# Kernel optimization log

Measured on AMD Instinct MI355X. Metric: run time of the kernel, lower is better.

The kernel has to match this reference:

```python
import jax, jax.numpy as jnp
import numpy as np

H = 8            # num heads
K_ORDER = 3      # polynomial filter order


def setup_inputs() -> dict:
    key = jax.random.key(0)
    ks = jax.random.split(key, 7)
    B, N, D = 4, 2048, 256
    s = 0.05  # weight scale to keep softmax/poly numerically tame
    x = jax.random.normal(ks[0], (B, N, D), jnp.float32)
    Wq = jax.random.normal(ks[1], (D, D), jnp.float32) * s
    Wk = jax.random.normal(ks[2], (D, D), jnp.float32) * s
    Wv = jax.random.normal(ks[3], (D, D), jnp.float32) * s
    Wo = jax.random.normal(ks[4], (D, D), jnp.float32) * s
    coeffs = jax.random.normal(ks[5], (H, K_ORDER + 1), jnp.float32) * 0.5
    z = jnp.zeros((D,), jnp.float32)
    return {"x": x, "Wq": Wq, "bq": z, "Wk": Wk, "bk": z,
            "Wv": Wv, "bv": z, "Wo": Wo, "bo": z, "coeffs": coeffs}


def reference(x, Wq, bq, Wk, bk, Wv, bv, Wo, bo, coeffs):
    B, N, D = x.shape
    hd = D // H

    def split_heads(t):  # [B,N,D] -> [B,H,N,hd]
        return t.reshape(B, N, H, hd).transpose(0, 2, 1, 3)

    q = split_heads(x @ Wq + bq)
    k = split_heads(x @ Wk + bk)
    v = split_heads(x @ Wv + bv)

    # Estimator: learned adjacency via scaled-dot-product softmax, [B,H,N,N]
    scale = jnp.asarray(1.0 / np.sqrt(hd), x.dtype)
    A = jax.nn.softmax(jnp.einsum('bhnd,bhmd->bhnm', q, k) * scale, axis=-1)

    # Filter: X' = sum_{k=0}^{K} c[h,k] * A^k V
    out = coeffs[None, :, 0, None, None] * v
    t = v
    for kk in range(1, K_ORDER + 1):
        t = jnp.einsum('bhnm,bhmd->bhnd', A, t)
        out = out + coeffs[None, :, kk, None, None] * t

    merged = out.transpose(0, 2, 1, 3).reshape(B, N, D)  # concat heads
    return merged @ Wo + bo
```

## Files before the change

kernel.cpp:

```cpp
#include <hip/hip_runtime.h>
#include <hip/hip_bf16.h>

typedef __hip_bfloat16 bf16;
typedef __attribute__((ext_vector_type(8))) short short8;
typedef __attribute__((ext_vector_type(4))) short short4v;
typedef __attribute__((ext_vector_type(4))) float f32x4;

#define BB 4
#define NN 2048
#define DD 256
#define HH 8
#define HD 32
#define BN (BB*NN)
#define ELEMS (BN*DD)

__device__ int g_isf32;
__device__ __attribute__((aligned(256))) unsigned short g_xb [ELEMS];
__device__ __attribute__((aligned(256))) unsigned short g_qb [ELEMS];
__device__ __attribute__((aligned(256))) unsigned short g_kb [ELEMS];
__device__ __attribute__((aligned(256))) unsigned short g_tA [ELEMS];
__device__ __attribute__((aligned(256))) unsigned short g_tB [ELEMS];
__device__ __attribute__((aligned(256))) float          g_acc[ELEMS];
__device__ __attribute__((aligned(256))) unsigned short g_mg [ELEMS];
__device__ __attribute__((aligned(256))) unsigned short g_wt [4*DD*DD];
__device__ __attribute__((aligned(256))) float g_bias[4*DD];
__device__ __attribute__((aligned(256))) float g_cf[HH*4];
__device__ __attribute__((aligned(256))) float g_invl[BB*HH*NN];

__device__ __forceinline__ float b2f(unsigned short u) {
    union { unsigned int i; float f; } c; c.i = ((unsigned int)u) << 16; return c.f;
}
__device__ __forceinline__ unsigned short f2b(float f) {
    bf16 h = __float2bfloat16(f);
    return *reinterpret_cast<unsigned short*>(&h);
}
#if __has_builtin(__builtin_amdgcn_cvt_pk_bf16_f32)
typedef __attribute__((ext_vector_type(2))) __bf16 bf16x2t;
__device__ __forceinline__ unsigned int pk2(float a, float b) {
    union { bf16x2t v; unsigned int u; } c;
    c.v = __builtin_amdgcn_cvt_pk_bf16_f32(a, b);
    return c.u;
}
#else
__device__ __forceinline__ unsigned int pk2(float a, float b) {
    unsigned int ua = __float_as_uint(a), ub = __float_as_uint(b);
    ua = (ua + 0x7FFFu + ((ua >> 16) & 1u)) >> 16;
    ub = (ub + 0x7FFFu + ((ub >> 16) & 1u)) & 0xFFFF0000u;
    return ua | ub;
}
#endif
__device__ __forceinline__ float ldin(const void* p, int i, int f32m) {
    return f32m ? ((const float*)p)[i] : b2f(((const unsigned short*)p)[i]);
}

__global__ __launch_bounds__(256) void probe_kernel(const void* __restrict__ x)
{
    __shared__ int cnt;
    if (threadIdx.x == 0) cnt = 0;
    __syncthreads();
    const unsigned short* u = (const unsigned short*)x;
    int w = 0;
    for (int i = threadIdx.x; i < 1024; i += 256) {
        const int e = (u[2 * i] >> 7) & 0xFF;
        if (e < 100 || e > 140) ++w;
    }
    atomicAdd(&cnt, w);
    __syncthreads();
    if (threadIdx.x == 0) g_isf32 = (cnt > 300) ? 1 : 0;
}

__global__ __launch_bounds__(256) void prep_x_kernel(const void* __restrict__ x)
{
    const int f32m = g_isf32;
    const size_t i0 = ((size_t)blockIdx.x * 256 + threadIdx.x) * 8;
    if (f32m) {
        const float4 a = *(const float4*)((const float*)x + i0);
        const float4 b = *(const float4*)((const float*)x + i0 + 4);
        union { uint4 v; unsigned int u[4]; } o;
        o.u[0] = pk2(a.x, a.y); o.u[1] = pk2(a.z, a.w);
        o.u[2] = pk2(b.x, b.y); o.u[3] = pk2(b.z, b.w);
        *(uint4*)(g_xb + i0) = o.v;
    } else {
        *(uint4*)(g_xb + i0) = *(const uint4*)((const unsigned short*)x + i0);
    }
}

__global__ __launch_bounds__(256) void prep_w_kernel(
    const void* W0, const void* W1, const void* W2, const void* W3,
    const void* bq, const void* bk, const void* bv, const void* bo,
    const void* coeffs)
{
    const int f32m = g_isf32;
    __shared__ unsigned short tile[64][65];
    const int mat = blockIdx.y;
    const void* W = (mat == 0) ? W0 : (mat == 1) ? W1 : (mat == 2) ? W2 : W3;
    const int k0 = (blockIdx.x >> 2) * 64;
    const int n0 = (blockIdx.x & 3) * 64;
    const int t  = threadIdx.x;

    if (blockIdx.x == 0 && blockIdx.y == 0) {
        g_bias[0 * DD + t] = ldin(bq, t, f32m);
        g_bias[1 * DD + t] = ldin(bk, t, f32m);
        g_bias[2 * DD + t] = ldin(bv, t, f32m);
        g_bias[3 * DD + t] = ldin(bo, t, f32m);
        if (t < 32) g_cf[t] = ldin(coeffs, t, f32m);
    }

    #pragma unroll
    for (int it = 0; it < 16; ++it) {
        const int flat = it * 256 + t;
        const int i = flat >> 6, j = flat & 63;
        tile[j][i] = f2b(ldin(W, (k0 + i) * DD + n0 + j, f32m));
    }
    __syncthreads();
    unsigned short* wt = g_wt + mat * DD * DD;
    #pragma unroll
    for (int it = 0; it < 16; ++it) {
        const int flat = it * 256 + t;
        const int nl = flat >> 6, kl = flat & 63;
        wt[(n0 + nl) * DD + k0 + kl] = tile[nl][kl];
    }
}

__global__ __launch_bounds__(256) void qkv_gemm_kernel()
{
    __shared__ unsigned short xs[128 * 32];
    __shared__ unsigned short wl[64 * 32];
    const int t  = threadIdx.x;
    const int w  = t >> 6, l = t & 63, lg = l >> 4, ln = l & 15;
    const int wm = w >> 1, wn = w & 1;
    const int r0 = blockIdx.x * 128;
    const int n0 = blockIdx.y * 64;
    const int mat = blockIdx.z;
    const unsigned short* wt = g_wt + mat * DD * DD;

    f32x4 acc[4][2];
    #pragma unroll
    for (int m = 0; m < 4; ++m)
        #pragma unroll
        for (int s = 0; s < 2; ++s) acc[m][s] = (f32x4){0,0,0,0};

    for (int kc = 0; kc < DD; kc += 32) {
        __syncthreads();
        #pragma unroll
        for (int c = 0; c < 2; ++c) {
            const int s = c * 256 + t;
            *(uint4*)(xs + (s >> 2) * 32 + (s & 3) * 8) =
                *(const uint4*)(g_xb + (size_t)(r0 + (s >> 2)) * DD + kc + (s & 3) * 8);
        }
        *(uint4*)(wl + (t >> 2) * 32 + (t & 3) * 8) =
            *(const uint4*)(wt + (size_t)(n0 + (t >> 2)) * DD + kc + (t & 3) * 8);
        __syncthreads();

        short8 af[4];
        #pragma unroll
        for (int m = 0; m < 4; ++m)
            af[m] = *(const short8*)(xs + (wm * 64 + m * 16 + ln) * 32 + lg * 8);
        #pragma unroll
        for (int s = 0; s < 2; ++s) {
            const short8 bfr = *(const short8*)(wl + (wn * 32 + s * 16 + ln) * 32 + lg * 8);
            #pragma unroll
            for (int m = 0; m < 4; ++m)
                acc[m][s] = __builtin_amdgcn_mfma_f32_16x16x32_bf16(af[m], bfr, acc[m][s], 0, 0, 0);
        }
    }

    const float QS = 0.17677669529663687f * 1.4426950408889634f;
    #pragma unroll
    for (int s = 0; s < 2; ++s) {
        const int j = n0 + wn * 32 + s * 16 + ln;
        const float bias = g_bias[mat * DD + j];
        const int h = j >> 5, dd = j & 31;
        #pragma unroll
        for (int m = 0; m < 4; ++m) {
            #pragma unroll
            for (int r = 0; r < 4; ++r) {
                const int rn = r0 + wm * 64 + m * 16 + lg * 4 + r;
                const int b = rn >> 11, n = rn & (NN - 1);
                const int bh = b * HH + h;
                const float val = acc[m][s][r] + bias;
                if (mat == 0) {
                    g_qb[((size_t)bh * NN + n) * HD + dd] = f2b(val * QS);
                } else if (mat == 1) {
                    g_kb[((size_t)bh * NN + n) * HD + dd] = f2b(val);
                } else {
                    g_tA[((size_t)bh * HD + dd) * NN + n] = f2b(val);
                    g_acc[(size_t)rn * DD + j] = g_cf[h * 4] * val;
                }
            }
        }
    }
}

#define KSP 40
#define TSP 136
template<int KIND>
__global__ __launch_bounds__(512, 1) void attn_pass_kernel(const int kidx, const int dir)
{
    __shared__ unsigned short ks[128 * KSP];
    __shared__ unsigned short ts[32 * TSP];

    const unsigned short* __restrict__ tin  = dir ? g_tB : g_tA;
    unsigned short*       __restrict__ tout = dir ? g_tA : g_tB;

    const int tid = threadIdx.x;
    const int w   = tid >> 6;
    const int l   = tid & 63;
    const int lg  = l >> 4;
    const int ln  = l & 15;

    const int bi = blockIdx.x;
    const int bh = (bi & 7) * 4 + ((bi >> 3) & 3);
    const int qt = bi >> 5;
    const int h  = bh & (HH - 1);
    const int b  = bh >> 3;
    const int q0 = qt * 128;
    const int qw = q0 + w * 16;

    const short8 qf = *(const short8*)(g_qb +
        ((size_t)bh * NN + qw + ln) * HD + lg * 8);

    const unsigned short* kb = g_kb + (size_t)bh * NN * HD;
    const unsigned short* tb = tin  + (size_t)bh * HD * NN;

    const f32x4 zero = {0.f, 0.f, 0.f, 0.f};
    f32x4 oacc0 = zero, oacc1 = zero;
    float lsum = 0.f;

    const int krow = tid >> 2, kcol = (tid & 3) * 8;
    const int trow = tid >> 4, tcol = (tid & 15) * 8;

    for (int it = 0; it < 16; ++it) {
        const int k0 = it * 128;
        __syncthreads();
        *(uint4*)(ks + krow * KSP + kcol) =
            *(const uint4*)(kb + (size_t)k0 * HD + tid * 8);
        *(uint4*)(ts + trow * TSP + tcol) =
            *(const uint4*)(tb + (size_t)trow * NN + k0 + tcol);
        __syncthreads();

        #pragma unroll
        for (int c = 0; c < 8; ++c) {
            const short8 kf = *(const short8*)(ks + (c * 16 + ln) * KSP + lg * 8);
            f32x4 s = __builtin_amdgcn_mfma_f32_16x16x32_bf16(kf, qf, zero, 0, 0, 0);
            float p[4];
            #pragma unroll
            for (int r = 0; r < 4; ++r) p[r] = __builtin_amdgcn_exp2f(s[r]);
            if (KIND == 0) lsum += p[0] + p[1] + p[2] + p[3];
            union { unsigned int u[2]; short4v s4; } pb;
            pb.u[0] = pk2(p[0], p[1]); pb.u[1] = pk2(p[2], p[3]);
            const short4v tf0 = *(const short4v*)(ts + ln * TSP + c * 16 + lg * 4);
            const short4v tf1 = *(const short4v*)(ts + (16 + ln) * TSP + c * 16 + lg * 4);
            oacc0 = __builtin_amdgcn_mfma_f32_16x16x16bf16_1k(tf0, pb.s4, oacc0, 0, 0, 0);
            oacc1 = __builtin_amdgcn_mfma_f32_16x16x16bf16_1k(tf1, pb.s4, oacc1, 0, 0, 0);
        }
    }

    float invl;
    if (KIND == 0) {
        lsum += __shfl_xor(lsum, 16, 64);
        lsum += __shfl_xor(lsum, 32, 64);
        invl = 1.0f / lsum;
        if (lg == 0) g_invl[(size_t)bh * NN + qw + ln] = invl;
    } else {
        invl = g_invl[(size_t)bh * NN + qw + ln];
    }

    const float ck = g_cf[h * 4 + kidx];
    #pragma unroll
    for (int hf = 0; hf < 2; ++hf) {
        const f32x4& oa = hf ? oacc1 : oacc0;
        #pragma unroll
        for (int r = 0; r < 4; ++r) {
            const int d = hf * 16 + lg * 4 + r;
            const float val = oa[r] * invl;
            const size_t gi = ((size_t)(b * NN + qw + ln)) * DD + h * HD + d;
            if (KIND != 2) {
                tout[((size_t)bh * HD + d) * NN + qw + ln] = f2b(val);
                g_acc[gi] += ck * val;
            } else {
                g_mg[gi] = f2b(g_acc[gi] + ck * val);
            }
        }
    }
}

__global__ __launch_bounds__(256) void out_gemm_kernel(void* __restrict__ out)
{
    __shared__ unsigned short xs[64 * 32];
    __shared__ unsigned short wl[64 * 32];
    const int f32m = g_isf32;
    const int t  = threadIdx.x;
    const int w  = t >> 6, l = t & 63, lg = l >> 4, ln = l & 15;
    const int r0 = blockIdx.x * 64;
    const int n0 = blockIdx.y * 64;
    const unsigned short* wt = g_wt + 3 * DD * DD;
    const int sr = t >> 2, sc = (t & 3) * 8;

    f32x4 acc[4] = {{0,0,0,0},{0,0,0,0},{0,0,0,0},{0,0,0,0}};

    for (int kc = 0; kc < DD; kc += 32) {
        __syncthreads();
        *(uint4*)(xs + sr * 32 + sc) =
            *(const uint4*)(g_mg + (size_t)(r0 + sr) * DD + kc + sc);
        *(uint4*)(wl + sr * 32 + sc) =
            *(const uint4*)(wt + (size_t)(n0 + sr) * DD + kc + sc);
        __syncthreads();
        const short8 af = *(const short8*)(xs + (w * 16 + ln) * 32 + lg * 8);
        #pragma unroll
        for (int s = 0; s < 4; ++s) {
            const short8 bfr = *(const short8*)(wl + (s * 16 + ln) * 32 + lg * 8);
            acc[s] = __builtin_amdgcn_mfma_f32_16x16x32_bf16(af, bfr, acc[s], 0, 0, 0);
        }
    }

    #pragma unroll
    for (int s = 0; s < 4; ++s) {
        const int j = n0 + s * 16 + ln;
        const float bias = g_bias[3 * DD + j];
        #pragma unroll
        for (int r = 0; r < 4; ++r) {
            const int rn = r0 + w * 16 + lg * 4 + r;
            const float val = acc[s][r] + bias;
            if (f32m) ((float*)out)[(size_t)rn * DD + j] = val;
            else      ((bf16*)out)[(size_t)rn * DD + j] = __float2bfloat16(val);
        }
    }
}

extern "C" void kernel_launch(void* const* d_in, const int* in_sizes, int n_in,
                              void* d_out, int out_size, void* d_ws, size_t ws_size,
                              hipStream_t stream)
{
    const void* x      = d_in[0];
    const void* Wq     = d_in[1];
    const void* bq     = d_in[2];
    const void* Wk     = d_in[3];
    const void* bk     = d_in[4];
    const void* Wv     = d_in[5];
    const void* bv     = d_in[6];
    const void* Wo     = d_in[7];
    const void* bo     = d_in[8];
    const void* coeffs = d_in[9];
    (void)d_ws; (void)ws_size; (void)in_sizes; (void)n_in; (void)out_size;

    probe_kernel<<<1, 256, 0, stream>>>(x);

    prep_x_kernel<<<ELEMS / (256 * 8), 256, 0, stream>>>(x);
    prep_w_kernel<<<dim3(16, 4), 256, 0, stream>>>(Wq, Wk, Wv, Wo,
                                                   bq, bk, bv, bo, coeffs);

    qkv_gemm_kernel<<<dim3(64, 4, 3), 256, 0, stream>>>();

    const int agrid = (BB * HH) * (NN / 128);
    attn_pass_kernel<0><<<agrid, 512, 0, stream>>>(1, 0);
    attn_pass_kernel<1><<<agrid, 512, 0, stream>>>(2, 1);
    attn_pass_kernel<2><<<agrid, 512, 0, stream>>>(3, 0);

    out_gemm_kernel<<<dim3(128, 4), 256, 0, stream>>>(d_out);
}
```

Before: 228.0 us.

## Double-buffer attention K/T tiles, batch MFMAs, and fuse probe into prep kernels

```diff
diff --git a/kernel.cpp b/kernel.cpp
--- a/kernel.cpp
+++ b/kernel.cpp
@@ -14,7 +14,6 @@
 #define BN (BB*NN)
 #define ELEMS (BN*DD)
 
-__device__ int g_isf32;
 __device__ __attribute__((aligned(256))) unsigned short g_xb [ELEMS];
 __device__ __attribute__((aligned(256))) unsigned short g_qb [ELEMS];
 __device__ __attribute__((aligned(256))) unsigned short g_kb [ELEMS];
@@ -53,52 +52,55 @@
     return f32m ? ((const float*)p)[i] : b2f(((const unsigned short*)p)[i]);
 }
 
-__global__ __launch_bounds__(256) void probe_kernel(const void* __restrict__ x)
+__device__ __forceinline__ int block_probe(const void* x, int tid, int nthr)
 {
     __shared__ int cnt;
-    if (threadIdx.x == 0) cnt = 0;
+    if (tid == 0) cnt = 0;
     __syncthreads();
     const unsigned short* u = (const unsigned short*)x;
     int w = 0;
-    for (int i = threadIdx.x; i < 1024; i += 256) {
+    for (int i = tid; i < 1024; i += nthr) {
         const int e = (u[2 * i] >> 7) & 0xFF;
         if (e < 100 || e > 140) ++w;
     }
-    atomicAdd(&cnt, w);
+    if (w) atomicAdd(&cnt, w);
     __syncthreads();
-    if (threadIdx.x == 0) g_isf32 = (cnt > 300) ? 1 : 0;
-}
-
-__global__ __launch_bounds__(256) void prep_x_kernel(const void* __restrict__ x)
-{
-    const int f32m = g_isf32;
-    const size_t i0 = ((size_t)blockIdx.x * 256 + threadIdx.x) * 8;
-    if (f32m) {
-        const float4 a = *(const float4*)((const float*)x + i0);
-        const float4 b = *(const float4*)((const float*)x + i0 + 4);
-        union { uint4 v; unsigned int u[4]; } o;
-        o.u[0] = pk2(a.x, a.y); o.u[1] = pk2(a.z, a.w);
-        o.u[2] = pk2(b.x, b.y); o.u[3] = pk2(b.z, b.w);
-        *(uint4*)(g_xb + i0) = o.v;
-    } else {
-        *(uint4*)(g_xb + i0) = *(const uint4*)((const unsigned short*)x + i0);
-    }
-}
-
-__global__ __launch_bounds__(256) void prep_w_kernel(
+    return cnt > 300;
+}
+
+__global__ __launch_bounds__(256) void prep_kernel(
+    const void* __restrict__ x,
     const void* W0, const void* W1, const void* W2, const void* W3,
     const void* bq, const void* bk, const void* bv, const void* bo,
     const void* coeffs)
 {
-    const int f32m = g_isf32;
+    const int t = threadIdx.x;
+    const int f32m = block_probe(x, t, 256);
+
+    if (blockIdx.x < 1024) {
+        const size_t i0 = ((size_t)blockIdx.x * 256 + t) * 8;
+        if (f32m) {
+            const float4 a = *(const float4*)((const float*)x + i0);
+            const float4 b = *(const float4*)((const float*)x + i0 + 4);
+            union { uint4 v; unsigned int u[4]; } o;
+            o.u[0] = pk2(a.x, a.y); o.u[1] = pk2(a.z, a.w);
+            o.u[2] = pk2(b.x, b.y); o.u[3] = pk2(b.z, b.w);
+            *(uint4*)(g_xb + i0) = o.v;
+        } else {
+            *(uint4*)(g_xb + i0) = *(const uint4*)((const unsigned short*)x + i0);
+        }
+        return;
+    }
+
     __shared__ unsigned short tile[64][65];
-    const int mat = blockIdx.y;
+    const int bi  = blockIdx.x - 1024;
+    const int mat = bi >> 4;
+    const int bx  = bi & 15;
     const void* W = (mat == 0) ? W0 : (mat == 1) ? W1 : (mat == 2) ? W2 : W3;
-    const int k0 = (blockIdx.x >> 2) * 64;
-    const int n0 = (blockIdx.x & 3) * 64;
-    const int t  = threadIdx.x;
-
-    if (blockIdx.x == 0 && blockIdx.y == 0) {
+    const int k0 = (bx >> 2) * 64;
+    const int n0 = (bx & 3) * 64;
+
+    if (bi == 0) {
         g_bias[0 * DD + t] = ldin(bq, t, f32m);
         g_bias[1 * DD + t] = ldin(bk, t, f32m);
         g_bias[2 * DD + t] = ldin(bv, t, f32m);
@@ -197,8 +199,8 @@
 template<int KIND>
 __global__ __launch_bounds__(512, 1) void attn_pass_kernel(const int kidx, const int dir)
 {
-    __shared__ unsigned short ks[128 * KSP];
-    __shared__ unsigned short ts[32 * TSP];
+    __shared__ unsigned short ks[2][128 * KSP];
+    __shared__ unsigned short ts[2][32 * TSP];
 
     const unsigned short* __restrict__ tin  = dir ? g_tB : g_tA;
     unsigned short*       __restrict__ tout = dir ? g_tA : g_tB;
@@ -224,37 +226,76 @@
     const unsigned short* tb = tin  + (size_t)bh * HD * NN;
 
     const f32x4 zero = {0.f, 0.f, 0.f, 0.f};
-    f32x4 oacc0 = zero, oacc1 = zero;
+    f32x4 o0e = zero, o0o = zero, o1e = zero, o1o = zero;
     float lsum = 0.f;
 
     const int krow = tid >> 2, kcol = (tid & 3) * 8;
     const int trow = tid >> 4, tcol = (tid & 15) * 8;
 
+    uint4 krg = *(const uint4*)(kb + tid * 8);
+    uint4 trg = *(const uint4*)(tb + (size_t)trow * NN + tcol);
+    *(uint4*)(ks[0] + krow * KSP + kcol) = krg;
+    *(uint4*)(ts[0] + trow * TSP + tcol) = trg;
+    __syncthreads();
+
+    int cur = 0;
     for (int it = 0; it < 16; ++it) {
-        const int k0 = it * 128;
+        if (it < 15) {
+            const int k1 = (it + 1) * 128;
+            krg = *(const uint4*)(kb + (size_t)k1 * HD + tid * 8);
+            trg = *(const uint4*)(tb + (size_t)trow * NN + k1 + tcol);
+        }
+        const unsigned short* ksc = ks[cur];
+        const unsigned short* tsc = ts[cur];
+
+        #pragma unroll
+        for (int half = 0; half < 2; ++half) {
+            short8 kf[4];
+            #pragma unroll
+            for (int c = 0; c < 4; ++c)
+                kf[c] = *(const short8*)(ksc + ((half * 4 + c) * 16 + ln) * KSP + lg * 8);
+            f32x4 s[4];
+            #pragma unroll
+            for (int c = 0; c < 4; ++c)
+                s[c] = __builtin_amdgcn_mfma_f32_16x16x32_bf16(kf[c], qf, zero, 0, 0, 0);
+            float p[16];
+            #pragma unroll
+            for (int c = 0; c < 4; ++c)
+                #pragma unroll
+                for (int r = 0; r < 4; ++r)
+                    p[c * 4 + r] = __builtin_amdgcn_exp2f(s[c][r]);
+            if (KIND == 0) {
+                #pragma unroll
+                for (int e = 0; e < 16; ++e) lsum += p[e];
+            }
+            #pragma unroll
+            for (int c = 0; c < 4; ++c) {
+                const int cc = half * 4 + c;
+                union { unsigned int u[2]; short4v s4; } pb;
+                pb.u[0] = pk2(p[c * 4 + 0], p[c * 4 + 1]);
+                pb.u[1] = pk2(p[c * 4 + 2], p[c * 4 + 3]);
+                const short4v tf0 = *(const short4v*)(tsc + ln * TSP + cc * 16 + lg * 4);
+                const short4v tf1 = *(const short4v*)(tsc + (16 + ln) * TSP + cc * 16 + lg * 4);
+                if (cc & 1) {
+                    o0o = __builtin_amdgcn_mfma_f32_16x16x16bf16_1k(tf0, pb.s4, o0o, 0, 0, 0);
+                    o1o = __builtin_amdgcn_mfma_f32_16x16x16bf16_1k(tf1, pb.s4, o1o, 0, 0, 0);
+                } else {
+                    o0e = __builtin_amdgcn_mfma_f32_16x16x16bf16_1k(tf0, pb.s4, o0e, 0, 0, 0);
+                    o1e = __builtin_amdgcn_mfma_f32_16x16x16bf16_1k(tf1, pb.s4, o1e, 0, 0, 0);
+                }
+            }
+        }
+
+        if (it < 15) {
+            *(uint4*)(ks[cur ^ 1] + krow * KSP + kcol) = krg;
+            *(uint4*)(ts[cur ^ 1] + trow * TSP + tcol) = trg;
+        }
         __syncthreads();
-        *(uint4*)(ks + krow * KSP + kcol) =
-            *(const uint4*)(kb + (size_t)k0 * HD + tid * 8);
-        *(uint4*)(ts + trow * TSP + tcol) =
-            *(const uint4*)(tb + (size_t)trow * NN + k0 + tcol);
-        __syncthreads();
-
-        #pragma unroll
-        for (int c = 0; c < 8; ++c) {
-            const short8 kf = *(const short8*)(ks + (c * 16 + ln) * KSP + lg * 8);
-            f32x4 s = __builtin_amdgcn_mfma_f32_16x16x32_bf16(kf, qf, zero, 0, 0, 0);
-            float p[4];
-            #pragma unroll
-            for (int r = 0; r < 4; ++r) p[r] = __builtin_amdgcn_exp2f(s[r]);
-            if (KIND == 0) lsum += p[0] + p[1] + p[2] + p[3];
-            union { unsigned int u[2]; short4v s4; } pb;
-            pb.u[0] = pk2(p[0], p[1]); pb.u[1] = pk2(p[2], p[3]);
-            const short4v tf0 = *(const short4v*)(ts + ln * TSP + c * 16 + lg * 4);
-            const short4v tf1 = *(const short4v*)(ts + (16 + ln) * TSP + c * 16 + lg * 4);
-            oacc0 = __builtin_amdgcn_mfma_f32_16x16x16bf16_1k(tf0, pb.s4, oacc0, 0, 0, 0);
-            oacc1 = __builtin_amdgcn_mfma_f32_16x16x16bf16_1k(tf1, pb.s4, oacc1, 0, 0, 0);
-        }
-    }
+        cur ^= 1;
+    }
+
+    const f32x4 oacc0 = o0e + o0o;
+    const f32x4 oacc1 = o1e + o1o;
 
     float invl;
     if (KIND == 0) {
@@ -285,12 +326,13 @@
     }
 }
 
-__global__ __launch_bounds__(256) void out_gemm_kernel(void* __restrict__ out)
-{
+__global__ __launch_bounds__(256) void out_gemm_kernel(void* __restrict__ out,
+                                                       const void* __restrict__ x)
+{
+    const int t  = threadIdx.x;
+    const int f32m = block_probe(x, t, 256);
     __shared__ unsigned short xs[64 * 32];
     __shared__ unsigned short wl[64 * 32];
-    const int f32m = g_isf32;
-    const int t  = threadIdx.x;
     const int w  = t >> 6, l = t & 63, lg = l >> 4, ln = l & 15;
     const int r0 = blockIdx.x * 64;
     const int n0 = blockIdx.y * 64;
@@ -344,11 +386,8 @@
     const void* coeffs = d_in[9];
     (void)d_ws; (void)ws_size; (void)in_sizes; (void)n_in; (void)out_size;
 
-    probe_kernel<<<1, 256, 0, stream>>>(x);
-
-    prep_x_kernel<<<ELEMS / (256 * 8), 256, 0, stream>>>(x);
-    prep_w_kernel<<<dim3(16, 4), 256, 0, stream>>>(Wq, Wk, Wv, Wo,
-                                                   bq, bk, bv, bo, coeffs);
+    prep_kernel<<<1088, 256, 0, stream>>>(x, Wq, Wk, Wv, Wo,
+                                          bq, bk, bv, bo, coeffs);
 
     qkv_gemm_kernel<<<dim3(64, 4, 3), 256, 0, stream>>>();
 
@@ -357,5 +396,5 @@
     attn_pass_kernel<1><<<agrid, 512, 0, stream>>>(2, 1);
     attn_pass_kernel<2><<<agrid, 512, 0, stream>>>(3, 0);
 
-    out_gemm_kernel<<<dim3(128, 4), 256, 0, stream>>>(d_out);
-}
+    out_gemm_kernel<<<dim3(128, 4), 256, 0, stream>>>(d_out, x);
+}
```

Measured after the change: 216.1 us. -5.2%, faster.
